# Optimization experiments

Hardware: AMD Instinct MI355X
Metric: run time of the kernel (lower is better)

The kernel has to match this reference:

```python
import jax, jax.numpy as jnp
import numpy as np
from jax import lax

B, T, MEL, D, H, NC = 8, 256, 128, 192, 4, 20
C_EVENT, C_SCENE = 8, 64
ETA, LR, ALPHA = 0.9, 0.1, 0.01  # memory momentum, write lr, forget rate
EPS = 1e-5


def _ln(x, g, b):
    m = x.mean(-1, keepdims=True)
    v = ((x - m) ** 2).mean(-1, keepdims=True)
    return (x - m) / jnp.sqrt(v + EPS) * g + b


def _mem_step(x, t, M, S, Wk, Wv, Wq, chunk):
    # x: [B,D]; M,S: [B,D,D]. Titans-style neural memory, updated every `chunk` steps.
    k = x @ Wk
    v = x @ Wv
    q = x @ Wq
    err = v - jnp.einsum('bd,bde->be', k, M)          # surprise / prediction error
    S_new = ETA * S + LR * jnp.einsum('bd,be->bde', k, err)
    M_new = (1.0 - ALPHA) * M + S_new
    upd = (t % chunk) == 0
    S = jnp.where(upd, S_new, S)
    M = jnp.where(upd, M_new, M)
    out = jnp.einsum('bd,bde->be', q, M)              # retrieval
    return out, M, S


def setup_inputs() -> dict:
    key = jax.random.key(0)
    ks = jax.random.split(key, 24)
    w = lambda k, shp, s=0.05: jax.random.normal(k, shp, dtype=jnp.float32) * s
    inp = {
        'x': jax.random.normal(ks[0], (B, T, MEL), dtype=jnp.float32),
        'W_in': w(ks[1], (MEL, D)), 'b_in': jnp.zeros((D,), jnp.float32),
        # MHA at seq_len=1: softmax over one key -> weight 1, so only V and out proj matter
        'Wv_a': w(ks[2], (D, D)), 'bv_a': jnp.zeros((D,), jnp.float32),
        'Wo_a': w(ks[3], (D, D)), 'bo_a': jnp.zeros((D,), jnp.float32),
        # conformer conv module (degenerate seq_len=1: depthwise conv -> center tap)
        'ln1_g': jnp.ones((D,), jnp.float32), 'ln1_b': jnp.zeros((D,), jnp.float32),
        'pw1_w': w(ks[4], (D, 2 * D)), 'pw1_b': jnp.zeros((2 * D,), jnp.float32),
        'dw_w': w(ks[5], (D,), 0.2), 'dw_b': jnp.zeros((D,), jnp.float32),
        'bn_s': jnp.ones((D,), jnp.float32), 'bn_b': jnp.zeros((D,), jnp.float32),
        'pw2_w': w(ks[6], (D, D)), 'pw2_b': jnp.zeros((D,), jnp.float32),
        # theta (event) / delta (scene) neural memory projections
        'Wk_t': w(ks[7], (D, D)), 'Wv_t': w(ks[8], (D, D)), 'Wq_t': w(ks[9], (D, D)),
        'Wk_d': w(ks[10], (D, D)), 'Wv_d': w(ks[11], (D, D)), 'Wq_d': w(ks[12], (D, D)),
        'ln2_g': jnp.ones((D,), jnp.float32), 'ln2_b': jnp.zeros((D,), jnp.float32),
        'Wc': w(ks[13], (D, NC)), 'bc': jnp.zeros((NC,), jnp.float32),
    }
    return inp


def reference(x, W_in, b_in, Wv_a, bv_a, Wo_a, bo_a, ln1_g, ln1_b, pw1_w, pw1_b,
              dw_w, dw_b, bn_s, bn_b, pw2_w, pw2_b, Wk_t, Wv_t, Wq_t,
              Wk_d, Wv_d, Wq_d, ln2_g, ln2_b, Wc, bc):
    xp = x @ W_in + b_in                               # [B,T,D]

    def step(carry, inp):
        x_t, t = inp                                   # x_t: [B,D]
        Mt, St, Md, Sd = carry
        d_out, Md, Sd = _mem_step(x_t, t, Md, Sd, Wk_d, Wv_d, Wq_d, C_SCENE)
        x1 = x_t + 0.5 * d_out
        attn = (x1 @ Wv_a + bv_a) @ Wo_a + bo_a        # single-token self-attn
        x2 = x1 + attn
        h = _ln(x2, ln1_g, ln1_b)
        h = h @ pw1_w + pw1_b
        a, g = jnp.split(h, 2, axis=-1)
        h = a * jax.nn.sigmoid(g)                      # GLU
        h = h * dw_w + dw_b                            # depthwise conv center tap
        h = h * bn_s + bn_b                            # eval-mode BN
        h = jax.nn.silu(h)
        h = h @ pw2_w + pw2_b
        x3 = x2 + h
        t_out, Mt, St = _mem_step(x3, t, Mt, St, Wk_t, Wv_t, Wq_t, C_EVENT)
        x4 = x3 + 0.5 * t_out
        return (Mt, St, Md, Sd), _ln(x4, ln2_g, ln2_b)

    z = jnp.zeros((B, D, D), jnp.float32)
    xs = (jnp.swapaxes(xp, 0, 1), jnp.arange(T))       # [T,B,D], [T]
    _, ys = lax.scan(step, (z, z, z, z), xs)
    y = jnp.swapaxes(ys, 0, 1)                         # [B,T,D]
    pooled = y.mean(axis=1)
    return pooled @ Wc + bc                            # [B,NC]
```

## Files before the change

### kernel.cpp

```cpp
#include <hip/hip_runtime.h>
#include <math.h>

#define Bb 8
#define Tt 256
#define MEL 128
#define Dd 192
#define NCc 20
#define ND 4
#define NT 32
#define ETAc 0.9f
#define LRc 0.1f
#define MDEC 0.99f
#define EPSc 1e-5f
#define PT 2
#define PTILES 128
#define RTT 4
#define PADD 196

__device__ __forceinline__ float sigmoidf_(float x) {
    return 1.0f / (1.0f + __expf(-x));
}

__device__ __forceinline__ float memcoef(int n, int i) {
    float m = LRc, pw = LRc;
    for (int nn = i + 1; nn <= n; nn++) { pw *= ETAc; m = MDEC * m + pw; }
    return m;
}

__device__ __forceinline__ float dot4(float4 a, float4 b) {
    return a.x * b.x + a.y * b.y + a.z * b.z + a.w * b.w;
}

__global__ __launch_bounds__(192) void prep(
    const float* __restrict__ Wv_a, const float* __restrict__ Wo_a,
    const float* __restrict__ bv_a, const float* __restrict__ bo_a,
    const float* __restrict__ Wq_t, const float* __restrict__ Wq_d,
    const float* __restrict__ x, const float* __restrict__ W_in,
    const float* __restrict__ b_in, const float* __restrict__ Wk_d,
    const float* __restrict__ Wv_d,
    float* __restrict__ Wavo_ws, float* __restrict__ b_avo,
    float* __restrict__ WqtT, float* __restrict__ WqdT,
    float* __restrict__ Kd_ws, float* __restrict__ Vd_ws,
    float* __restrict__ pooled)
{
    __shared__ __align__(16) float smem[768];
    int blk = blockIdx.x, tid = threadIdx.x;

    if (blk < 48) {
        int m0 = blk * 4;
        for (int q = tid; q < 4 * Dd; q += 192) smem[q] = Wv_a[m0 * Dd + q];
        __syncthreads();
        int o = tid;
        float a0 = 0.f, a1 = 0.f, a2 = 0.f, a3 = 0.f;
        #pragma unroll 4
        for (int k = 0; k < Dd; k += 2) {
            float w0 = Wo_a[(k + 0) * Dd + o], w1 = Wo_a[(k + 1) * Dd + o];
            a0 += w0 * smem[0 * Dd + k] + w1 * smem[0 * Dd + k + 1];
            a1 += w0 * smem[1 * Dd + k] + w1 * smem[1 * Dd + k + 1];
            a2 += w0 * smem[2 * Dd + k] + w1 * smem[2 * Dd + k + 1];
            a3 += w0 * smem[3 * Dd + k] + w1 * smem[3 * Dd + k + 1];
        }
        Wavo_ws[(m0 + 0) * Dd + o] = a0;
        Wavo_ws[(m0 + 1) * Dd + o] = a1;
        Wavo_ws[(m0 + 2) * Dd + o] = a2;
        Wavo_ws[(m0 + 3) * Dd + o] = a3;
        return;
    }
    if (blk == 48) {
        int o = tid;
        float s = bo_a[o];
        #pragma unroll 4
        for (int m = 0; m < Dd; m++) s += bv_a[m] * Wo_a[m * Dd + o];
        b_avo[o] = s;
        return;
    }
    if (blk < 97) {
        int r0 = 4 * (blk - 49);
        float4 v;
        v.x = Wq_t[(r0 + 0) * Dd + tid];
        v.y = Wq_t[(r0 + 1) * Dd + tid];
        v.z = Wq_t[(r0 + 2) * Dd + tid];
        v.w = Wq_t[(r0 + 3) * Dd + tid];
        *(float4*)&WqtT[tid * Dd + r0] = v;
        return;
    }
    if (blk < 145) {
        int r0 = 4 * (blk - 97);
        float4 v;
        v.x = Wq_d[(r0 + 0) * Dd + tid];
        v.y = Wq_d[(r0 + 1) * Dd + tid];
        v.z = Wq_d[(r0 + 2) * Dd + tid];
        v.w = Wq_d[(r0 + 3) * Dd + tid];
        *(float4*)&WqdT[tid * Dd + r0] = v;
        return;
    }
    if (blk == 177) {
        for (int q = tid; q < Bb * Dd; q += 192) pooled[q] = 0.f;
        return;
    }

    int q = blk - 145;
    int b = q >> 2, i = q & 3;
    float* XR = smem;
    float* XP = smem + 128;
    if (tid < 128) XR[tid] = x[((size_t)b * Tt + 64 * i) * MEL + tid];
    __syncthreads();
    {
        int o = tid;
        float acc = b_in[o];
        #pragma unroll 8
        for (int k = 0; k < MEL; k += 4) {
            acc += W_in[(k + 0) * Dd + o] * XR[k + 0];
            acc += W_in[(k + 1) * Dd + o] * XR[k + 1];
            acc += W_in[(k + 2) * Dd + o] * XR[k + 2];
            acc += W_in[(k + 3) * Dd + o] * XR[k + 3];
        }
        XP[o] = acc;
    }
    __syncthreads();
    {
        int o = tid;
        float ak = 0.f, av = 0.f;
        #pragma unroll 4
        for (int k = 0; k < Dd; k += 4) {
            float x0 = XP[k + 0], x1 = XP[k + 1], x2 = XP[k + 2], x3 = XP[k + 3];
            ak += Wk_d[(k + 0) * Dd + o] * x0 + Wk_d[(k + 1) * Dd + o] * x1
                + Wk_d[(k + 2) * Dd + o] * x2 + Wk_d[(k + 3) * Dd + o] * x3;
            av += Wv_d[(k + 0) * Dd + o] * x0 + Wv_d[(k + 1) * Dd + o] * x1
                + Wv_d[(k + 2) * Dd + o] * x2 + Wv_d[(k + 3) * Dd + o] * x3;
        }
        Kd_ws[(b * ND + i) * Dd + o] = ak;
        Vd_ws[(b * ND + i) * Dd + o] = av;
    }
}

__global__ __launch_bounds__(192) void delta_solve(
    const float* __restrict__ WqdT, const float* __restrict__ Kd_ws,
    float* __restrict__ Vd_ws, float* __restrict__ Ud_ws)
{
    int blk = blockIdx.x, b = blk / 5, role = blk % 5, tid = threadIdx.x;
    if (role == 0) {
        __shared__ __align__(16) float K4[ND][Dd], V4[ND][Dd];
        __shared__ float G[16], mc[16];
        for (int q = tid; q < ND * 48; q += 192) {
            int i = q / 48, c = q - i * 48;
            ((float4*)K4[i])[c] = ((const float4*)&Kd_ws[(b * ND + i) * Dd])[c];
            ((float4*)V4[i])[c] = ((const float4*)&Vd_ws[(b * ND + i) * Dd])[c];
        }
        __syncthreads();
        if (tid < 16) {
            int i = tid >> 2, j = tid & 3;
            float s = 0.f;
            for (int d = 0; d < Dd; d++) s += K4[i][d] * K4[j][d];
            G[tid] = s;
            mc[tid] = (j <= i) ? memcoef(i, j) : 0.f;
        }
        __syncthreads();
        for (int i = 1; i < ND; i++) {
            float acc = V4[i][tid];
            for (int m = 0; m < i; m++)
                acc -= mc[(i - 1) * ND + m] * G[i * ND + m] * V4[m][tid];
            V4[i][tid] = acc;
            __syncthreads();
        }
        for (int i = 0; i < ND; i++) Vd_ws[(b * ND + i) * Dd + tid] = V4[i][tid];
    } else {
        __shared__ float KS[Dd];
        int i = role - 1;
        KS[tid] = Kd_ws[(b * ND + i) * Dd + tid];
        __syncthreads();
        int o = tid;
        float acc = 0.f;
        #pragma unroll 8
        for (int k = 0; k < Dd; k += 4) {
            acc += WqdT[(k + 0) * Dd + o] * KS[k + 0];
            acc += WqdT[(k + 1) * Dd + o] * KS[k + 1];
            acc += WqdT[(k + 2) * Dd + o] * KS[k + 2];
            acc += WqdT[(k + 3) * Dd + o] * KS[k + 3];
        }
        Ud_ws[(b * ND + i) * Dd + o] = acc;
    }
}

__global__ __launch_bounds__(192) void pipeline(
    const float* __restrict__ x, const float* __restrict__ W_in,
    const float* __restrict__ b_in,
    const float* __restrict__ ln1_g, const float* __restrict__ ln1_b,
    const float* __restrict__ pw1_w, const float* __restrict__ pw1_b,
    const float* __restrict__ dw_w, const float* __restrict__ dw_b,
    const float* __restrict__ bn_s, const float* __restrict__ bn_b,
    const float* __restrict__ pw2_w, const float* __restrict__ pw2_b,
    const float* __restrict__ Wavo_ws, const float* __restrict__ b_avo,
    const float* __restrict__ Ed_ws, const float* __restrict__ Ud_ws,
    float* __restrict__ x3_ws)
{
    int blk = blockIdx.x;
    int b = blk >> 7, tile = blk & 127;
    int t0 = tile * PT, n = tile >> 5;
    int tid = threadIdx.x;

    __shared__ __align__(16) float XR[PT][MEL];
    __shared__ __align__(16) float XP[PT][Dd];
    __shared__ __align__(16) float ED[ND][PADD], UD[ND][PADD];
    __shared__ __align__(16) float X1[PT][Dd], X2[PT][Dd];
    __shared__ __align__(16) float LNX[PT][Dd], HG[PT][Dd];
    __shared__ float WQs[PT * ND];
    __shared__ float mv[PT][2];

    if (tid < PT * 32) {
        int r = tid >> 5, c = tid & 31;
        ((float4*)XR[r])[c] = ((const float4*)&x[((size_t)b * Tt + t0 + r) * MEL])[c];
    }
    for (int q = tid; q < ND * 48 * 2; q += 192) {
        int which = q >= ND * 48;
        int qq = which ? q - ND * 48 : q;
        int i = qq / 48, c = qq - i * 48;
        if (!which) ((float4*)ED[i])[c] = ((const float4*)&Ed_ws[(b * ND + i) * Dd])[c];
        else        ((float4*)UD[i])[c] = ((const float4*)&Ud_ws[(b * ND + i) * Dd])[c];
    }
    __syncthreads();

    int o = tid;
    {
        float acc[PT];
        float bb = b_in[o];
        #pragma unroll
        for (int r = 0; r < PT; r++) acc[r] = bb;
        #pragma unroll 8
        for (int k = 0; k < MEL; k += 4) {
            float w0 = W_in[(k + 0) * Dd + o], w1 = W_in[(k + 1) * Dd + o];
            float w2 = W_in[(k + 2) * Dd + o], w3 = W_in[(k + 3) * Dd + o];
            #pragma unroll
            for (int r = 0; r < PT; r++) {
                float4 xv = *(const float4*)&XR[r][k];
                acc[r] += w0 * xv.x + w1 * xv.y + w2 * xv.z + w3 * xv.w;
            }
        }
        #pragma unroll
        for (int r = 0; r < PT; r++) XP[r][tid] = acc[r];
    }
    __syncthreads();

    if (tid < PT * 32) {
        int r = tid >> 5, i = (tid >> 3) & 3, c = tid & 7;
        float s = 0.f;
        const float* xp = XP[r];
        const float* u = UD[i];
        #pragma unroll
        for (int j = 0; j < 24; j++) s += xp[c * 24 + j] * u[c * 24 + j];
        s += __shfl_down(s, 4, 8);
        s += __shfl_down(s, 2, 8);
        s += __shfl_down(s, 1, 8);
        if (c == 0) {
            float coef = (i <= n) ? memcoef(n, i) : 0.f;
            WQs[r * ND + i] = s * coef;
        }
    }
    __syncthreads();

    {
        #pragma unroll
        for (int r = 0; r < PT; r++) {
            float dout = WQs[r * ND + 0] * ED[0][tid] + WQs[r * ND + 1] * ED[1][tid]
                       + WQs[r * ND + 2] * ED[2][tid] + WQs[r * ND + 3] * ED[3][tid];
            X1[r][tid] = XP[r][tid] + 0.5f * dout;
        }
    }
    __syncthreads();

    {
        float acc[PT];
        float bb = b_avo[o];
        #pragma unroll
        for (int r = 0; r < PT; r++) acc[r] = bb;
        #pragma unroll 8
        for (int k = 0; k < Dd; k += 4) {
            float w0 = Wavo_ws[(k + 0) * Dd + o], w1 = Wavo_ws[(k + 1) * Dd + o];
            float w2 = Wavo_ws[(k + 2) * Dd + o], w3 = Wavo_ws[(k + 3) * Dd + o];
            #pragma unroll
            for (int r = 0; r < PT; r++) {
                float4 xv = *(const float4*)&X1[r][k];
                acc[r] += w0 * xv.x + w1 * xv.y + w2 * xv.z + w3 * xv.w;
            }
        }
        #pragma unroll
        for (int r = 0; r < PT; r++) X2[r][tid] = X1[r][tid] + acc[r];
    }
    __syncthreads();

    if (tid < PT * 32) {
        int r = tid >> 5, j = tid & 31;
        float s = 0.f, sq = 0.f;
        for (int d = j; d < Dd; d += 32) { float v = X2[r][d]; s += v; sq += v * v; }
        for (int off = 16; off > 0; off >>= 1) {
            s += __shfl_down(s, off, 32); sq += __shfl_down(sq, off, 32);
        }
        if (j == 0) {
            float mean = s / Dd;
            mv[r][0] = mean;
            mv[r][1] = rsqrtf(sq / Dd - mean * mean + EPSc);
        }
    }
    __syncthreads();
    {
        float g = ln1_g[tid], bb = ln1_b[tid];
        #pragma unroll
        for (int r = 0; r < PT; r++)
            LNX[r][tid] = (X2[r][tid] - mv[r][0]) * mv[r][1] * g + bb;
    }
    __syncthreads();

    {
        float aa[PT], gg[PT];
        float ba = pw1_b[o], bg = pw1_b[o + Dd];
        #pragma unroll
        for (int r = 0; r < PT; r++) { aa[r] = ba; gg[r] = bg; }
        #pragma unroll 4
        for (int k = 0; k < Dd; k += 4) {
            float wa0 = pw1_w[(k + 0) * 2 * Dd + o], wg0 = pw1_w[(k + 0) * 2 * Dd + Dd + o];
            float wa1 = pw1_w[(k + 1) * 2 * Dd + o], wg1 = pw1_w[(k + 1) * 2 * Dd + Dd + o];
            float wa2 = pw1_w[(k + 2) * 2 * Dd + o], wg2 = pw1_w[(k + 2) * 2 * Dd + Dd + o];
            float wa3 = pw1_w[(k + 3) * 2 * Dd + o], wg3 = pw1_w[(k + 3) * 2 * Dd + Dd + o];
            #pragma unroll
            for (int r = 0; r < PT; r++) {
                float4 xv = *(const float4*)&LNX[r][k];
                aa[r] += wa0 * xv.x + wa1 * xv.y + wa2 * xv.z + wa3 * xv.w;
                gg[r] += wg0 * xv.x + wg1 * xv.y + wg2 * xv.z + wg3 * xv.w;
            }
        }
        float dww = dw_w[o], dwb = dw_b[o], bns = bn_s[o], bnb = bn_b[o];
        #pragma unroll
        for (int r = 0; r < PT; r++) {
            float h = aa[r] * sigmoidf_(gg[r]);
            h = h * dww + dwb;
            h = h * bns + bnb;
            h = h * sigmoidf_(h);
            HG[r][tid] = h;
        }
    }
    __syncthreads();

    {
        float acc[PT];
        float bb = pw2_b[o];
        #pragma unroll
        for (int r = 0; r < PT; r++) acc[r] = bb;
        #pragma unroll 8
        for (int k = 0; k < Dd; k += 4) {
            float w0 = pw2_w[(k + 0) * Dd + o], w1 = pw2_w[(k + 1) * Dd + o];
            float w2 = pw2_w[(k + 2) * Dd + o], w3 = pw2_w[(k + 3) * Dd + o];
            #pragma unroll
            for (int r = 0; r < PT; r++) {
                float4 xv = *(const float4*)&HG[r][k];
                acc[r] += w0 * xv.x + w1 * xv.y + w2 * xv.z + w3 * xv.w;
            }
        }
        #pragma unroll
        for (int r = 0; r < PT; r++)
            x3_ws[((size_t)b * Tt + t0 + r) * Dd + tid] = X2[r][tid] + acc[r];
    }
}

__global__ __launch_bounds__(192) void theta_projU(
    const float* __restrict__ x3_ws,
    const float* __restrict__ Wk_t, const float* __restrict__ Wv_t,
    const float* __restrict__ WqtT,
    float* __restrict__ Kt_ws, float* __restrict__ Vt_ws,
    float* __restrict__ Ut_ws)
{
    int blk = blockIdx.x, b = blk >> 5, i = blk & 31;
    int tid = threadIdx.x;
    __shared__ float XS[Dd];
    __shared__ float KS[Dd];

    XS[tid] = x3_ws[((size_t)b * Tt + 8 * i) * Dd + tid];
    __syncthreads();

    int o = tid;
    float ak = 0.f, av = 0.f;
    #pragma unroll 4
    for (int k = 0; k < Dd; k += 4) {
        float x0 = XS[k + 0], x1 = XS[k + 1], x2 = XS[k + 2], x3 = XS[k + 3];
        ak += Wk_t[(k + 0) * Dd + o] * x0 + Wk_t[(k + 1) * Dd + o] * x1
            + Wk_t[(k + 2) * Dd + o] * x2 + Wk_t[(k + 3) * Dd + o] * x3;
        av += Wv_t[(k + 0) * Dd + o] * x0 + Wv_t[(k + 1) * Dd + o] * x1
            + Wv_t[(k + 2) * Dd + o] * x2 + Wv_t[(k + 3) * Dd + o] * x3;
    }
    Kt_ws[(b * NT + i) * Dd + o] = ak;
    Vt_ws[(b * NT + i) * Dd + o] = av;
    KS[o] = ak;
    __syncthreads();

    float au = 0.f;
    #pragma unroll 8
    for (int k = 0; k < Dd; k += 4) {
        au += WqtT[(k + 0) * Dd + o] * KS[k + 0];
        au += WqtT[(k + 1) * Dd + o] * KS[k + 1];
        au += WqtT[(k + 2) * Dd + o] * KS[k + 2];
        au += WqtT[(k + 3) * Dd + o] * KS[k + 3];
    }
    Ut_ws[(b * NT + i) * Dd + o] = au;
}

__global__ __launch_bounds__(192) void theta_solve(
    const float* __restrict__ Kt_ws, float* __restrict__ Vt_ws)
{
    int b = blockIdx.x, tid = threadIdx.x;
    __shared__ __align__(16) float K[NT][PADD];
    __shared__ float A[NT * NT], mc[NT * NT];

    for (int q = tid; q < NT * 48; q += 192) {
        int i = q / 48, c = q - i * 48;
        ((float4*)K[i])[c] = ((const float4*)&Kt_ws[(b * NT + i) * Dd])[c];
    }
    if (tid < NT) {
        int i = tid;
        float m = 0.f, pw = LRc;
        for (int nn = 0; nn < NT; nn++) {
            float v;
            if (nn < i) v = 0.f;
            else if (nn == i) { m = LRc; v = m; }
            else { pw *= ETAc; m = MDEC * m + pw; v = m; }
            mc[nn * NT + i] = v;
        }
    }
    __syncthreads();
    for (int p = tid; p < NT * NT; p += 192) {
        int i = p >> 5, j = p & 31;
        float s = 0.f;
        if (j < i) {
            const float4* ki = (const float4*)K[i];
            const float4* kj = (const float4*)K[j];
            float g = 0.f;
            #pragma unroll 4
            for (int kk = 0; kk < 48; kk++) g += dot4(ki[kk], kj[kk]);
            s = mc[(i - 1) * NT + j] * g;
        }
        A[p] = s;
    }
    __syncthreads();
    float e[NT];
    #pragma unroll
    for (int i = 0; i < NT; i++) e[i] = Vt_ws[(b * NT + i) * Dd + tid];
    #pragma unroll
    for (int i = 1; i < NT; i++) {
        float acc = e[i];
        #pragma unroll
        for (int m = 0; m < i; m++) acc -= A[i * NT + m] * e[m];
        e[i] = acc;
    }
    #pragma unroll
    for (int i = 0; i < NT; i++) Vt_ws[(b * NT + i) * Dd + tid] = e[i];
}

__global__ __launch_bounds__(256) void retrieve(
    const float* __restrict__ x3_ws, const float* __restrict__ Ut_ws,
    const float* __restrict__ Et_ws, const float* __restrict__ ln2_g,
    const float* __restrict__ ln2_b, float* __restrict__ pooled)
{
    int blk = blockIdx.x, b = blk >> 6, tile = blk & 63;
    int t0 = tile * RTT, n = tile >> 1;
    int tid = threadIdx.x;

    __shared__ __align__(16) float UT[NT][PADD];
    __shared__ __align__(16) float XS[RTT][PADD];
    __shared__ float WQ[RTT * NT];
    __shared__ float mv[RTT][2];

    for (int q = tid; q < NT * 48; q += 256) {
        int i = q / 48, c = q - i * 48;
        ((float4*)UT[i])[c] = ((const float4*)&Ut_ws[(b * NT + i) * Dd])[c];
    }
    for (int q = tid; q < RTT * 48; q += 256) {
        int r = q / 48, c = q - r * 48;
        ((float4*)XS[r])[c] = ((const float4*)&x3_ws[((size_t)b * Tt + t0 + r) * Dd])[c];
    }
    __syncthreads();

    {
        int r = tid >> 6, i = (tid >> 1) & 31, h = tid & 1;
        const float4* u4 = (const float4*)UT[i];
        const float4* x4 = (const float4*)XS[r];
        float s = 0.f;
        #pragma unroll 8
        for (int kk = h * 24; kk < h * 24 + 24; kk++) s += dot4(u4[kk], x4[kk]);
        s += __shfl_down(s, 1, 2);
        if (h == 0) {
            float coef = (i <= n) ? memcoef(n, i) : 0.f;
            WQ[r * NT + i] = s * coef;
        }
    }
    __syncthreads();

    if (tid < Dd) {
        float acc[RTT] = {};
        #pragma unroll 4
        for (int i = 0; i < NT; i++) {
            float e = Et_ws[(b * NT + i) * Dd + tid];
            #pragma unroll
            for (int r = 0; r < RTT; r++) acc[r] += WQ[r * NT + i] * e;
        }
        #pragma unroll
        for (int r = 0; r < RTT; r++) XS[r][tid] += 0.5f * acc[r];
    }
    __syncthreads();

    if (tid < RTT * 32) {
        int r = tid >> 5, j = tid & 31;
        float s = 0.f, sq = 0.f;
        for (int d = j; d < Dd; d += 32) { float v = XS[r][d]; s += v; sq += v * v; }
        for (int off = 16; off > 0; off >>= 1) {
            s += __shfl_down(s, off, 32); sq += __shfl_down(sq, off, 32);
        }
        if (j == 0) {
            float mean = s / Dd;
            mv[r][0] = mean;
            mv[r][1] = rsqrtf(sq / Dd - mean * mean + EPSc);
        }
    }
    __syncthreads();

    if (tid < Dd) {
        float g = ln2_g[tid], bb = ln2_b[tid];
        float sum = 0.f;
        #pragma unroll
        for (int r = 0; r < RTT; r++)
            sum += (XS[r][tid] - mv[r][0]) * mv[r][1] * g + bb;
        atomicAdd(&pooled[b * Dd + tid], sum);
    }
}

__global__ __launch_bounds__(192) void head(
    const float* __restrict__ pooled, const float* __restrict__ Wc,
    const float* __restrict__ bc, float* __restrict__ out)
{
    int tid = threadIdx.x;
    if (tid < Bb * NCc) {
        int b = tid / NCc, c = tid - b * NCc;
        float s = 0.f;
        for (int d = 0; d < Dd; d++) s += pooled[b * Dd + d] * Wc[d * NCc + c];
        out[tid] = s * (1.0f / Tt) + bc[c];
    }
}

extern "C" void kernel_launch(void* const* d_in, const int* in_sizes, int n_in,
                              void* d_out, int out_size, void* d_ws, size_t ws_size,
                              hipStream_t stream) {
    const float* x     = (const float*)d_in[0];
    const float* W_in  = (const float*)d_in[1];
    const float* b_in  = (const float*)d_in[2];
    const float* Wv_a  = (const float*)d_in[3];
    const float* bv_a  = (const float*)d_in[4];
    const float* Wo_a  = (const float*)d_in[5];
    const float* bo_a  = (const float*)d_in[6];
    const float* ln1_g = (const float*)d_in[7];
    const float* ln1_b = (const float*)d_in[8];
    const float* pw1_w = (const float*)d_in[9];
    const float* pw1_b = (const float*)d_in[10];
    const float* dw_w  = (const float*)d_in[11];
    const float* dw_b  = (const float*)d_in[12];
    const float* bn_s  = (const float*)d_in[13];
    const float* bn_b  = (const float*)d_in[14];
    const float* pw2_w = (const float*)d_in[15];
    const float* pw2_b = (const float*)d_in[16];
    const float* Wk_t  = (const float*)d_in[17];
    const float* Wv_t  = (const float*)d_in[18];
    const float* Wq_t  = (const float*)d_in[19];
    const float* Wk_d  = (const float*)d_in[20];
    const float* Wv_d  = (const float*)d_in[21];
    const float* Wq_d  = (const float*)d_in[22];
    const float* ln2_g = (const float*)d_in[23];
    const float* ln2_b = (const float*)d_in[24];
    const float* Wc    = (const float*)d_in[25];
    const float* bc    = (const float*)d_in[26];

    float* ws = (float*)d_ws;
    size_t off = 0;
    float* x3_ws   = ws + off; off += (size_t)Bb * Tt * Dd;
    float* Kd_ws   = ws + off; off += Bb * ND * Dd;
    float* Vd_ws   = ws + off; off += Bb * ND * Dd;
    float* Ud_ws   = ws + off; off += Bb * ND * Dd;
    float* Kt_ws   = ws + off; off += Bb * NT * Dd;
    float* Vt_ws   = ws + off; off += Bb * NT * Dd;
    float* Ut_ws   = ws + off; off += Bb * NT * Dd;
    float* pooled  = ws + off; off += Bb * Dd;
    float* Wavo_ws = ws + off; off += Dd * Dd;
    float* WqtT    = ws + off; off += Dd * Dd;
    float* WqdT    = ws + off; off += Dd * Dd;
    float* b_avo   = ws + off; off += Dd;

    prep<<<178, 192, 0, stream>>>(
        Wv_a, Wo_a, bv_a, bo_a, Wq_t, Wq_d,
        x, W_in, b_in, Wk_d, Wv_d,
        Wavo_ws, b_avo, WqtT, WqdT, Kd_ws, Vd_ws, pooled);
    delta_solve<<<Bb * 5, 192, 0, stream>>>(WqdT, Kd_ws, Vd_ws, Ud_ws);
    pipeline<<<Bb * PTILES, 192, 0, stream>>>(
        x, W_in, b_in, ln1_g, ln1_b, pw1_w, pw1_b, dw_w, dw_b,
        bn_s, bn_b, pw2_w, pw2_b, Wavo_ws, b_avo, Vd_ws, Ud_ws, x3_ws);
    theta_projU<<<Bb * NT, 192, 0, stream>>>(
        x3_ws, Wk_t, Wv_t, WqtT, Kt_ws, Vt_ws, Ut_ws);
    theta_solve<<<Bb, 192, 0, stream>>>(Kt_ws, Vt_ws);
    retrieve<<<Bb * 64, 256, 0, stream>>>(
        x3_ws, Ut_ws, Vt_ws, ln2_g, ln2_b, pooled);
    head<<<1, 192, 0, stream>>>(pooled, Wc, bc, (float*)d_out);
}
```

Before: 195.2 us.

## Split-K across two thread halves in pipeline and theta kernels, double rows per tile

```diff
diff --git a/kernel.cpp b/kernel.cpp
--- a/kernel.cpp
+++ b/kernel.cpp
@@ -12,8 +12,8 @@
 #define LRc 0.1f
 #define MDEC 0.99f
 #define EPSc 1e-5f
-#define PT 2
-#define PTILES 128
+#define PT 4
+#define PTILES 64
 #define RTT 4
 #define PADD 196
 
@@ -182,7 +182,7 @@
     }
 }
 
-__global__ __launch_bounds__(192) void pipeline(
+__global__ __launch_bounds__(384) void pipeline(
     const float* __restrict__ x, const float* __restrict__ W_in,
     const float* __restrict__ b_in,
     const float* __restrict__ ln1_g, const float* __restrict__ ln1_b,
@@ -195,15 +195,18 @@
     float* __restrict__ x3_ws)
 {
     int blk = blockIdx.x;
-    int b = blk >> 7, tile = blk & 127;
-    int t0 = tile * PT, n = tile >> 5;
+    int b = blk >> 6, tile = blk & 63;
+    int t0 = tile * PT, n = tile >> 4;
     int tid = threadIdx.x;
+    int h = (tid >= Dd) ? 1 : 0;
+    int o = tid - h * Dd;
 
     __shared__ __align__(16) float XR[PT][MEL];
     __shared__ __align__(16) float XP[PT][Dd];
     __shared__ __align__(16) float ED[ND][PADD], UD[ND][PADD];
     __shared__ __align__(16) float X1[PT][Dd], X2[PT][Dd];
     __shared__ __align__(16) float LNX[PT][Dd], HG[PT][Dd];
+    __shared__ __align__(16) float PS[PT][Dd];
     __shared__ float WQs[PT * ND];
     __shared__ float mv[PT][2];
 
@@ -211,7 +214,7 @@
         int r = tid >> 5, c = tid & 31;
         ((float4*)XR[r])[c] = ((const float4*)&x[((size_t)b * Tt + t0 + r) * MEL])[c];
     }
-    for (int q = tid; q < ND * 48 * 2; q += 192) {
+    for (int q = tid; q < ND * 48 * 2; q += 384) {
         int which = q >= ND * 48;
         int qq = which ? q - ND * 48 : q;
         int i = qq / 48, c = qq - i * 48;
@@ -220,14 +223,11 @@
     }
     __syncthreads();
 
-    int o = tid;
-    {
-        float acc[PT];
-        float bb = b_in[o];
-        #pragma unroll
-        for (int r = 0; r < PT; r++) acc[r] = bb;
-        #pragma unroll 8
-        for (int k = 0; k < MEL; k += 4) {
+    {
+        float acc[PT] = {0.f, 0.f, 0.f, 0.f};
+        int k0 = h * 64;
+        #pragma unroll 4
+        for (int k = k0; k < k0 + 64; k += 4) {
             float w0 = W_in[(k + 0) * Dd + o], w1 = W_in[(k + 1) * Dd + o];
             float w2 = W_in[(k + 2) * Dd + o], w3 = W_in[(k + 3) * Dd + o];
             #pragma unroll
@@ -236,10 +236,18 @@
                 acc[r] += w0 * xv.x + w1 * xv.y + w2 * xv.z + w3 * xv.w;
             }
         }
-        #pragma unroll
-        for (int r = 0; r < PT; r++) XP[r][tid] = acc[r];
-    }
-    __syncthreads();
+        if (h) {
+            #pragma unroll
+            for (int r = 0; r < PT; r++) PS[r][o] = acc[r];
+        }
+        __syncthreads();
+        if (!h) {
+            float bb = b_in[o];
+            #pragma unroll
+            for (int r = 0; r < PT; r++) XP[r][o] = acc[r] + PS[r][o] + bb;
+        }
+        __syncthreads();
+    }
 
     if (tid < PT * 32) {
         int r = tid >> 5, i = (tid >> 3) & 3, c = tid & 7;
@@ -260,21 +268,20 @@
 
     {
         #pragma unroll
-        for (int r = 0; r < PT; r++) {
-            float dout = WQs[r * ND + 0] * ED[0][tid] + WQs[r * ND + 1] * ED[1][tid]
-                       + WQs[r * ND + 2] * ED[2][tid] + WQs[r * ND + 3] * ED[3][tid];
-            X1[r][tid] = XP[r][tid] + 0.5f * dout;
-        }
-    }
-    __syncthreads();
-
-    {
-        float acc[PT];
-        float bb = b_avo[o];
-        #pragma unroll
-        for (int r = 0; r < PT; r++) acc[r] = bb;
-        #pragma unroll 8
-        for (int k = 0; k < Dd; k += 4) {
+        for (int rr = 0; rr < 2; rr++) {
+            int r = h * 2 + rr;
+            float dout = WQs[r * ND + 0] * ED[0][o] + WQs[r * ND + 1] * ED[1][o]
+                       + WQs[r * ND + 2] * ED[2][o] + WQs[r * ND + 3] * ED[3][o];
+            X1[r][o] = XP[r][o] + 0.5f * dout;
+        }
+    }
+    __syncthreads();
+
+    {
+        float acc[PT] = {0.f, 0.f, 0.f, 0.f};
+        int k0 = h * 96;
+        #pragma unroll 4
+        for (int k = k0; k < k0 + 96; k += 4) {
             float w0 = Wavo_ws[(k + 0) * Dd + o], w1 = Wavo_ws[(k + 1) * Dd + o];
             float w2 = Wavo_ws[(k + 2) * Dd + o], w3 = Wavo_ws[(k + 3) * Dd + o];
             #pragma unroll
@@ -283,10 +290,18 @@
                 acc[r] += w0 * xv.x + w1 * xv.y + w2 * xv.z + w3 * xv.w;
             }
         }
-        #pragma unroll
-        for (int r = 0; r < PT; r++) X2[r][tid] = X1[r][tid] + acc[r];
-    }
-    __syncthreads();
+        if (h) {
+            #pragma unroll
+            for (int r = 0; r < PT; r++) PS[r][o] = acc[r];
+        }
+        __syncthreads();
+        if (!h) {
+            float bb = b_avo[o];
+            #pragma unroll
+            for (int r = 0; r < PT; r++) X2[r][o] = X1[r][o] + acc[r] + PS[r][o] + bb;
+        }
+        __syncthreads();
+    }
 
     if (tid < PT * 32) {
         int r = tid >> 5, j = tid & 31;
@@ -303,50 +318,55 @@
     }
     __syncthreads();
     {
-        float g = ln1_g[tid], bb = ln1_b[tid];
-        #pragma unroll
-        for (int r = 0; r < PT; r++)
-            LNX[r][tid] = (X2[r][tid] - mv[r][0]) * mv[r][1] * g + bb;
-    }
-    __syncthreads();
-
-    {
-        float aa[PT], gg[PT];
-        float ba = pw1_b[o], bg = pw1_b[o + Dd];
-        #pragma unroll
-        for (int r = 0; r < PT; r++) { aa[r] = ba; gg[r] = bg; }
+        float g = ln1_g[o], bb = ln1_b[o];
+        #pragma unroll
+        for (int rr = 0; rr < 2; rr++) {
+            int r = h * 2 + rr;
+            LNX[r][o] = (X2[r][o] - mv[r][0]) * mv[r][1] * g + bb;
+        }
+    }
+    __syncthreads();
+
+    {
+        int oc = h ? (Dd + o) : o;
+        float acc[PT];
+        float bb = pw1_b[oc];
+        #pragma unroll
+        for (int r = 0; r < PT; r++) acc[r] = bb;
         #pragma unroll 4
         for (int k = 0; k < Dd; k += 4) {
-            float wa0 = pw1_w[(k + 0) * 2 * Dd + o], wg0 = pw1_w[(k + 0) * 2 * Dd + Dd + o];
-            float wa1 = pw1_w[(k + 1) * 2 * Dd + o], wg1 = pw1_w[(k + 1) * 2 * Dd + Dd + o];
-            float wa2 = pw1_w[(k + 2) * 2 * Dd + o], wg2 = pw1_w[(k + 2) * 2 * Dd + Dd + o];
-            float wa3 = pw1_w[(k + 3) * 2 * Dd + o], wg3 = pw1_w[(k + 3) * 2 * Dd + Dd + o];
+            float w0 = pw1_w[(k + 0) * 2 * Dd + oc], w1 = pw1_w[(k + 1) * 2 * Dd + oc];
+            float w2 = pw1_w[(k + 2) * 2 * Dd + oc], w3 = pw1_w[(k + 3) * 2 * Dd + oc];
             #pragma unroll
             for (int r = 0; r < PT; r++) {
                 float4 xv = *(const float4*)&LNX[r][k];
-                aa[r] += wa0 * xv.x + wa1 * xv.y + wa2 * xv.z + wa3 * xv.w;
-                gg[r] += wg0 * xv.x + wg1 * xv.y + wg2 * xv.z + wg3 * xv.w;
+                acc[r] += w0 * xv.x + w1 * xv.y + w2 * xv.z + w3 * xv.w;
             }
         }
-        float dww = dw_w[o], dwb = dw_b[o], bns = bn_s[o], bnb = bn_b[o];
-        #pragma unroll
-        for (int r = 0; r < PT; r++) {
-            float h = aa[r] * sigmoidf_(gg[r]);
-            h = h * dww + dwb;
-            h = h * bns + bnb;
-            h = h * sigmoidf_(h);
-            HG[r][tid] = h;
-        }
-    }
-    __syncthreads();
-
-    {
-        float acc[PT];
-        float bb = pw2_b[o];
-        #pragma unroll
-        for (int r = 0; r < PT; r++) acc[r] = bb;
-        #pragma unroll 8
-        for (int k = 0; k < Dd; k += 4) {
+        if (h) {
+            #pragma unroll
+            for (int r = 0; r < PT; r++) PS[r][o] = acc[r];
+        }
+        __syncthreads();
+        if (!h) {
+            float dww = dw_w[o], dwb = dw_b[o], bns = bn_s[o], bnb = bn_b[o];
+            #pragma unroll
+            for (int r = 0; r < PT; r++) {
+                float hh = acc[r] * sigmoidf_(PS[r][o]);
+                hh = hh * dww + dwb;
+                hh = hh * bns + bnb;
+                hh = hh * sigmoidf_(hh);
+                HG[r][o] = hh;
+            }
+        }
+        __syncthreads();
+    }
+
+    {
+        float acc[PT] = {0.f, 0.f, 0.f, 0.f};
+        int k0 = h * 96;
+        #pragma unroll 4
+        for (int k = k0; k < k0 + 96; k += 4) {
             float w0 = pw2_w[(k + 0) * Dd + o], w1 = pw2_w[(k + 1) * Dd + o];
             float w2 = pw2_w[(k + 2) * Dd + o], w3 = pw2_w[(k + 3) * Dd + o];
             #pragma unroll
@@ -355,13 +375,21 @@
                 acc[r] += w0 * xv.x + w1 * xv.y + w2 * xv.z + w3 * xv.w;
             }
         }
-        #pragma unroll
-        for (int r = 0; r < PT; r++)
-            x3_ws[((size_t)b * Tt + t0 + r) * Dd + tid] = X2[r][tid] + acc[r];
-    }
-}
-
-__global__ __launch_bounds__(192) void theta_projU(
+        if (h) {
+            #pragma unroll
+            for (int r = 0; r < PT; r++) PS[r][o] = acc[r];
+        }
+        __syncthreads();
+        if (!h) {
+            float bb = pw2_b[o];
+            #pragma unroll
+            for (int r = 0; r < PT; r++)
+                x3_ws[((size_t)b * Tt + t0 + r) * Dd + o] = X2[r][o] + acc[r] + PS[r][o] + bb;
+        }
+    }
+}
+
+__global__ __launch_bounds__(384) void theta_projU(
     const float* __restrict__ x3_ws,
     const float* __restrict__ Wk_t, const float* __restrict__ Wv_t,
     const float* __restrict__ WqtT,
@@ -370,46 +398,47 @@
 {
     int blk = blockIdx.x, b = blk >> 5, i = blk & 31;
     int tid = threadIdx.x;
-    __shared__ float XS[Dd];
-    __shared__ float KS[Dd];
-
-    XS[tid] = x3_ws[((size_t)b * Tt + 8 * i) * Dd + tid];
-    __syncthreads();
-
-    int o = tid;
-    float ak = 0.f, av = 0.f;
+    int h = (tid >= Dd) ? 1 : 0;
+    int o = tid - h * Dd;
+    __shared__ __align__(16) float XS[Dd];
+    __shared__ __align__(16) float KS[Dd];
+    __shared__ __align__(16) float PS[Dd];
+
+    if (tid < 48)
+        ((float4*)XS)[tid] = ((const float4*)&x3_ws[((size_t)b * Tt + 8 * i) * Dd])[tid];
+    __syncthreads();
+
+    const float* W = h ? Wv_t : Wk_t;
+    float a = 0.f;
     #pragma unroll 4
     for (int k = 0; k < Dd; k += 4) {
-        float x0 = XS[k + 0], x1 = XS[k + 1], x2 = XS[k + 2], x3 = XS[k + 3];
-        ak += Wk_t[(k + 0) * Dd + o] * x0 + Wk_t[(k + 1) * Dd + o] * x1
-            + Wk_t[(k + 2) * Dd + o] * x2 + Wk_t[(k + 3) * Dd + o] * x3;
-        av += Wv_t[(k + 0) * Dd + o] * x0 + Wv_t[(k + 1) * Dd + o] * x1
-            + Wv_t[(k + 2) * Dd + o] * x2 + Wv_t[(k + 3) * Dd + o] * x3;
-    }
-    Kt_ws[(b * NT + i) * Dd + o] = ak;
-    Vt_ws[(b * NT + i) * Dd + o] = av;
-    KS[o] = ak;
+        a += W[(k + 0) * Dd + o] * XS[k + 0] + W[(k + 1) * Dd + o] * XS[k + 1]
+           + W[(k + 2) * Dd + o] * XS[k + 2] + W[(k + 3) * Dd + o] * XS[k + 3];
+    }
+    if (!h) { Kt_ws[(b * NT + i) * Dd + o] = a; KS[o] = a; }
+    else    { Vt_ws[(b * NT + i) * Dd + o] = a; }
     __syncthreads();
 
     float au = 0.f;
-    #pragma unroll 8
-    for (int k = 0; k < Dd; k += 4) {
-        au += WqtT[(k + 0) * Dd + o] * KS[k + 0];
-        au += WqtT[(k + 1) * Dd + o] * KS[k + 1];
-        au += WqtT[(k + 2) * Dd + o] * KS[k + 2];
-        au += WqtT[(k + 3) * Dd + o] * KS[k + 3];
-    }
-    Ut_ws[(b * NT + i) * Dd + o] = au;
-}
-
-__global__ __launch_bounds__(192) void theta_solve(
+    int k0 = h * 96;
+    #pragma unroll 4
+    for (int k = k0; k < k0 + 96; k += 4) {
+        au += WqtT[(k + 0) * Dd + o] * KS[k + 0] + WqtT[(k + 1) * Dd + o] * KS[k + 1]
+            + WqtT[(k + 2) * Dd + o] * KS[k + 2] + WqtT[(k + 3) * Dd + o] * KS[k + 3];
+    }
+    if (h) PS[o] = au;
+    __syncthreads();
+    if (!h) Ut_ws[(b * NT + i) * Dd + o] = au + PS[o];
+}
+
+__global__ __launch_bounds__(512) void theta_solve(
     const float* __restrict__ Kt_ws, float* __restrict__ Vt_ws)
 {
     int b = blockIdx.x, tid = threadIdx.x;
     __shared__ __align__(16) float K[NT][PADD];
     __shared__ float A[NT * NT], mc[NT * NT];
 
-    for (int q = tid; q < NT * 48; q += 192) {
+    for (int q = tid; q < NT * 48; q += 512) {
         int i = q / 48, c = q - i * 48;
         ((float4*)K[i])[c] = ((const float4*)&Kt_ws[(b * NT + i) * Dd])[c];
     }
@@ -425,7 +454,7 @@
         }
     }
     __syncthreads();
-    for (int p = tid; p < NT * NT; p += 192) {
+    for (int p = tid; p < NT * NT; p += 512) {
         int i = p >> 5, j = p & 31;
         float s = 0.f;
         if (j < i) {
@@ -439,18 +468,20 @@
         A[p] = s;
     }
     __syncthreads();
-    float e[NT];
-    #pragma unroll
-    for (int i = 0; i < NT; i++) e[i] = Vt_ws[(b * NT + i) * Dd + tid];
-    #pragma unroll
-    for (int i = 1; i < NT; i++) {
-        float acc = e[i];
-        #pragma unroll
-        for (int m = 0; m < i; m++) acc -= A[i * NT + m] * e[m];
-        e[i] = acc;
-    }
-    #pragma unroll
-    for (int i = 0; i < NT; i++) Vt_ws[(b * NT + i) * Dd + tid] = e[i];
+    if (tid < Dd) {
+        float e[NT];
+        #pragma unroll
+        for (int i = 0; i < NT; i++) e[i] = Vt_ws[(b * NT + i) * Dd + tid];
+        #pragma unroll
+        for (int i = 1; i < NT; i++) {
+            float acc = e[i];
+            #pragma unroll
+            for (int m = 0; m < i; m++) acc -= A[i * NT + m] * e[m];
+            e[i] = acc;
+        }
+        #pragma unroll
+        for (int i = 0; i < NT; i++) Vt_ws[(b * NT + i) * Dd + tid] = e[i];
+    }
 }
 
 __global__ __launch_bounds__(256) void retrieve(
@@ -594,12 +625,12 @@
         x, W_in, b_in, Wk_d, Wv_d,
         Wavo_ws, b_avo, WqtT, WqdT, Kd_ws, Vd_ws, pooled);
     delta_solve<<<Bb * 5, 192, 0, stream>>>(WqdT, Kd_ws, Vd_ws, Ud_ws);
-    pipeline<<<Bb * PTILES, 192, 0, stream>>>(
+    pipeline<<<Bb * PTILES, 384, 0, stream>>>(
         x, W_in, b_in, ln1_g, ln1_b, pw1_w, pw1_b, dw_w, dw_b,
         bn_s, bn_b, pw2_w, pw2_b, Wavo_ws, b_avo, Vd_ws, Ud_ws, x3_ws);
-    theta_projU<<<Bb * NT, 192, 0, stream>>>(
+    theta_projU<<<Bb * NT, 384, 0, stream>>>(
         x3_ws, Wk_t, Wv_t, WqtT, Kt_ws, Vt_ws, Ut_ws);
-    theta_solve<<<Bb, 192, 0, stream>>>(Kt_ws, Vt_ws);
+    theta_solve<<<Bb, 512, 0, stream>>>(Kt_ws, Vt_ws);
     retrieve<<<Bb * 64, 256, 0, stream>>>(
         x3_ws, Ut_ws, Vt_ws, ln2_g, ln2_b, pooled);
     head<<<1, 192, 0, stream>>>(pooled, Wc, bc, (float*)d_out);
```

Result: slower. 204.2 us (+4.6%).

## Fuse theta solve and head into preceding kernels via last-block atomic counters

Applied to the files above, without the earlier changes.

```diff
diff --git a/kernel.cpp b/kernel.cpp
--- a/kernel.cpp
+++ b/kernel.cpp
@@ -41,7 +41,7 @@
     float* __restrict__ Wavo_ws, float* __restrict__ b_avo,
     float* __restrict__ WqtT, float* __restrict__ WqdT,
     float* __restrict__ Kd_ws, float* __restrict__ Vd_ws,
-    float* __restrict__ pooled)
+    float* __restrict__ pooled, unsigned int* __restrict__ cnt)
 {
     __shared__ __align__(16) float smem[768];
     int blk = blockIdx.x, tid = threadIdx.x;
@@ -96,6 +96,7 @@
     }
     if (blk == 177) {
         for (int q = tid; q < Bb * Dd; q += 192) pooled[q] = 0.f;
+        if (tid < 12) cnt[tid] = 0u;
         return;
     }
 
@@ -361,102 +362,109 @@
     }
 }
 
-__global__ __launch_bounds__(192) void theta_projU(
+__global__ __launch_bounds__(384) void theta_projU_solve(
     const float* __restrict__ x3_ws,
     const float* __restrict__ Wk_t, const float* __restrict__ Wv_t,
     const float* __restrict__ WqtT,
     float* __restrict__ Kt_ws, float* __restrict__ Vt_ws,
-    float* __restrict__ Ut_ws)
+    float* __restrict__ Ut_ws, unsigned int* __restrict__ cnt)
 {
     int blk = blockIdx.x, b = blk >> 5, i = blk & 31;
     int tid = threadIdx.x;
-    __shared__ float XS[Dd];
-    __shared__ float KS[Dd];
-
-    XS[tid] = x3_ws[((size_t)b * Tt + 8 * i) * Dd + tid];
-    __syncthreads();
-
-    int o = tid;
-    float ak = 0.f, av = 0.f;
+    int h = (tid >= Dd) ? 1 : 0;
+    int o = tid - h * Dd;
+    __shared__ __align__(16) float XS[Dd];
+    __shared__ __align__(16) float KS[Dd];
+    __shared__ __align__(16) float PS[Dd];
+
+    if (tid < 48)
+        ((float4*)XS)[tid] = ((const float4*)&x3_ws[((size_t)b * Tt + 8 * i) * Dd])[tid];
+    __syncthreads();
+
+    const float* W = h ? Wv_t : Wk_t;
+    float a = 0.f;
     #pragma unroll 4
     for (int k = 0; k < Dd; k += 4) {
-        float x0 = XS[k + 0], x1 = XS[k + 1], x2 = XS[k + 2], x3 = XS[k + 3];
-        ak += Wk_t[(k + 0) * Dd + o] * x0 + Wk_t[(k + 1) * Dd + o] * x1
-            + Wk_t[(k + 2) * Dd + o] * x2 + Wk_t[(k + 3) * Dd + o] * x3;
-        av += Wv_t[(k + 0) * Dd + o] * x0 + Wv_t[(k + 1) * Dd + o] * x1
-            + Wv_t[(k + 2) * Dd + o] * x2 + Wv_t[(k + 3) * Dd + o] * x3;
-    }
-    Kt_ws[(b * NT + i) * Dd + o] = ak;
-    Vt_ws[(b * NT + i) * Dd + o] = av;
-    KS[o] = ak;
+        a += W[(k + 0) * Dd + o] * XS[k + 0] + W[(k + 1) * Dd + o] * XS[k + 1]
+           + W[(k + 2) * Dd + o] * XS[k + 2] + W[(k + 3) * Dd + o] * XS[k + 3];
+    }
+    if (!h) { Kt_ws[(b * NT + i) * Dd + o] = a; KS[o] = a; }
+    else    { Vt_ws[(b * NT + i) * Dd + o] = a; }
     __syncthreads();
 
     float au = 0.f;
-    #pragma unroll 8
-    for (int k = 0; k < Dd; k += 4) {
-        au += WqtT[(k + 0) * Dd + o] * KS[k + 0];
-        au += WqtT[(k + 1) * Dd + o] * KS[k + 1];
-        au += WqtT[(k + 2) * Dd + o] * KS[k + 2];
-        au += WqtT[(k + 3) * Dd + o] * KS[k + 3];
-    }
-    Ut_ws[(b * NT + i) * Dd + o] = au;
-}
-
-__global__ __launch_bounds__(192) void theta_solve(
-    const float* __restrict__ Kt_ws, float* __restrict__ Vt_ws)
-{
-    int b = blockIdx.x, tid = threadIdx.x;
+    int k0 = h * 96;
+    #pragma unroll 4
+    for (int k = k0; k < k0 + 96; k += 4) {
+        au += WqtT[(k + 0) * Dd + o] * KS[k + 0] + WqtT[(k + 1) * Dd + o] * KS[k + 1]
+            + WqtT[(k + 2) * Dd + o] * KS[k + 2] + WqtT[(k + 3) * Dd + o] * KS[k + 3];
+    }
+    if (h) PS[o] = au;
+    __syncthreads();
+    if (!h) Ut_ws[(b * NT + i) * Dd + o] = au + PS[o];
+
+    __syncthreads();
+    __shared__ unsigned int sdone;
+    if (tid == 0) { __threadfence(); sdone = atomicAdd(&cnt[b], 1u); }
+    __syncthreads();
+    if (sdone != 31u) return;
+    __threadfence();
+
     __shared__ __align__(16) float K[NT][PADD];
     __shared__ float A[NT * NT], mc[NT * NT];
 
-    for (int q = tid; q < NT * 48; q += 192) {
-        int i = q / 48, c = q - i * 48;
-        ((float4*)K[i])[c] = ((const float4*)&Kt_ws[(b * NT + i) * Dd])[c];
+    for (int q = tid; q < NT * 48; q += 384) {
+        int ii = q / 48, c = q - ii * 48;
+        ((float4*)K[ii])[c] = ((const float4*)&Kt_ws[(b * NT + ii) * Dd])[c];
     }
     if (tid < NT) {
-        int i = tid;
+        int ii = tid;
         float m = 0.f, pw = LRc;
         for (int nn = 0; nn < NT; nn++) {
             float v;
-            if (nn < i) v = 0.f;
-            else if (nn == i) { m = LRc; v = m; }
+            if (nn < ii) v = 0.f;
+            else if (nn == ii) { m = LRc; v = m; }
             else { pw *= ETAc; m = MDEC * m + pw; v = m; }
-            mc[nn * NT + i] = v;
-        }
-    }
-    __syncthreads();
-    for (int p = tid; p < NT * NT; p += 192) {
-        int i = p >> 5, j = p & 31;
+            mc[nn * NT + ii] = v;
+        }
+    }
+    __syncthreads();
+    for (int p = tid; p < NT * NT; p += 384) {
+        int ii = p >> 5, j = p & 31;
         float s = 0.f;
-        if (j < i) {
-            const float4* ki = (const float4*)K[i];
+        if (j < ii) {
+            const float4* ki = (const float4*)K[ii];
             const float4* kj = (const float4*)K[j];
             float g = 0.f;
             #pragma unroll 4
             for (int kk = 0; kk < 48; kk++) g += dot4(ki[kk], kj[kk]);
-            s = mc[(i - 1) * NT + j] * g;
+            s = mc[(ii - 1) * NT + j] * g;
         }
         A[p] = s;
     }
     __syncthreads();
-    float e[NT];
-    #pragma unroll
-    for (int i = 0; i < NT; i++) e[i] = Vt_ws[(b * NT + i) * Dd + tid];
-    #pragma unroll
-    for (int i = 1; i < NT; i++) {
-        float acc = e[i];
-        #pragma unroll
-        for (int m = 0; m < i; m++) acc -= A[i * NT + m] * e[m];
-        e[i] = acc;
-    }
-    #pragma unroll
-    for (int i = 0; i < NT; i++) Vt_ws[(b * NT + i) * Dd + tid] = e[i];
+    if (tid < Dd) {
+        float e[NT];
+        #pragma unroll
+        for (int ii = 0; ii < NT; ii++) e[ii] = Vt_ws[(b * NT + ii) * Dd + tid];
+        #pragma unroll
+        for (int ii = 1; ii < NT; ii++) {
+            float acc = e[ii];
+            #pragma unroll
+            for (int m = 0; m < ii; m++) acc -= A[ii * NT + m] * e[m];
+            e[ii] = acc;
+        }
+        #pragma unroll
+        for (int ii = 0; ii < NT; ii++) Vt_ws[(b * NT + ii) * Dd + tid] = e[ii];
+    }
 }
 
 __global__ __launch_bounds__(256) void retrieve(
     const float* __restrict__ x3_ws, const float* __restrict__ Ut_ws,
     const float* __restrict__ Et_ws, const float* __restrict__ ln2_g,
-    const float* __restrict__ ln2_b, float* __restrict__ pooled)
+    const float* __restrict__ ln2_b, float* __restrict__ pooled,
+    const float* __restrict__ Wc, const float* __restrict__ bc,
+    float* __restrict__ out, unsigned int* __restrict__ cnt)
 {
     int blk = blockIdx.x, b = blk >> 6, tile = blk & 63;
     int t0 = tile * RTT, n = tile >> 1;
@@ -528,17 +536,18 @@
             sum += (XS[r][tid] - mv[r][0]) * mv[r][1] * g + bb;
         atomicAdd(&pooled[b * Dd + tid], sum);
     }
-}
-
-__global__ __launch_bounds__(192) void head(
-    const float* __restrict__ pooled, const float* __restrict__ Wc,
-    const float* __restrict__ bc, float* __restrict__ out)
-{
-    int tid = threadIdx.x;
+
+    __syncthreads();
+    __shared__ unsigned int sdone;
+    if (tid == 0) { __threadfence(); sdone = atomicAdd(&cnt[8], 1u); }
+    __syncthreads();
+    if (sdone != (unsigned)(Bb * 64 - 1)) return;
+    __threadfence();
+
     if (tid < Bb * NCc) {
-        int b = tid / NCc, c = tid - b * NCc;
+        int b2 = tid / NCc, c = tid - b2 * NCc;
         float s = 0.f;
-        for (int d = 0; d < Dd; d++) s += pooled[b * Dd + d] * Wc[d * NCc + c];
+        for (int d = 0; d < Dd; d++) s += pooled[b2 * Dd + d] * Wc[d * NCc + c];
         out[tid] = s * (1.0f / Tt) + bc[c];
     }
 }
@@ -588,19 +597,18 @@
     float* WqtT    = ws + off; off += Dd * Dd;
     float* WqdT    = ws + off; off += Dd * Dd;
     float* b_avo   = ws + off; off += Dd;
+    unsigned int* cnt = (unsigned int*)(ws + off); off += 16;
 
     prep<<<178, 192, 0, stream>>>(
         Wv_a, Wo_a, bv_a, bo_a, Wq_t, Wq_d,
         x, W_in, b_in, Wk_d, Wv_d,
-        Wavo_ws, b_avo, WqtT, WqdT, Kd_ws, Vd_ws, pooled);
+        Wavo_ws, b_avo, WqtT, WqdT, Kd_ws, Vd_ws, pooled, cnt);
     delta_solve<<<Bb * 5, 192, 0, stream>>>(WqdT, Kd_ws, Vd_ws, Ud_ws);
     pipeline<<<Bb * PTILES, 192, 0, stream>>>(
         x, W_in, b_in, ln1_g, ln1_b, pw1_w, pw1_b, dw_w, dw_b,
         bn_s, bn_b, pw2_w, pw2_b, Wavo_ws, b_avo, Vd_ws, Ud_ws, x3_ws);
-    theta_projU<<<Bb * NT, 192, 0, stream>>>(
-        x3_ws, Wk_t, Wv_t, WqtT, Kt_ws, Vt_ws, Ut_ws);
-    theta_solve<<<Bb, 192, 0, stream>>>(Kt_ws, Vt_ws);
+    theta_projU_solve<<<Bb * NT, 384, 0, stream>>>(
+        x3_ws, Wk_t, Wv_t, WqtT, Kt_ws, Vt_ws, Ut_ws, cnt);
     retrieve<<<Bb * 64, 256, 0, stream>>>(
-        x3_ws, Ut_ws, Vt_ws, ln2_g, ln2_b, pooled);
-    head<<<1, 192, 0, stream>>>(pooled, Wc, bc, (float*)d_out);
-}
+        x3_ws, Ut_ws, Vt_ws, ln2_g, ln2_b, pooled, Wc, bc, (float*)d_out, cnt);
+}
```

Measured after the change: 202.0 us. 1.03x slower.

## Fuse theta projections into pipeline kernel and widen solve blocks

Applied to the files above, without the earlier changes.

```diff
diff --git a/kernel.cpp b/kernel.cpp
--- a/kernel.cpp
+++ b/kernel.cpp
@@ -148,11 +148,19 @@
             ((float4*)V4[i])[c] = ((const float4*)&Vd_ws[(b * ND + i) * Dd])[c];
         }
         __syncthreads();
+        if (tid < 128) {
+            int p = tid >> 3, c = tid & 7;
+            int i = p >> 2, j = p & 3;
+            float s = 0.f;
+            #pragma unroll
+            for (int d = c * 24; d < c * 24 + 24; d++) s += K4[i][d] * K4[j][d];
+            s += __shfl_down(s, 4, 8);
+            s += __shfl_down(s, 2, 8);
+            s += __shfl_down(s, 1, 8);
+            if (c == 0) G[p] = s;
+        }
         if (tid < 16) {
             int i = tid >> 2, j = tid & 3;
-            float s = 0.f;
-            for (int d = 0; d < Dd; d++) s += K4[i][d] * K4[j][d];
-            G[tid] = s;
             mc[tid] = (j <= i) ? memcoef(i, j) : 0.f;
         }
         __syncthreads();
@@ -192,7 +200,11 @@
     const float* __restrict__ pw2_w, const float* __restrict__ pw2_b,
     const float* __restrict__ Wavo_ws, const float* __restrict__ b_avo,
     const float* __restrict__ Ed_ws, const float* __restrict__ Ud_ws,
-    float* __restrict__ x3_ws)
+    const float* __restrict__ Wk_t, const float* __restrict__ Wv_t,
+    const float* __restrict__ WqtT,
+    float* __restrict__ x3_ws,
+    float* __restrict__ Kt_ws, float* __restrict__ Vt_ws,
+    float* __restrict__ Ut_ws)
 {
     int blk = blockIdx.x;
     int b = blk >> 7, tile = blk & 127;
@@ -340,6 +352,7 @@
     }
     __syncthreads();
 
+    float x3v0;
     {
         float acc[PT];
         float bb = pw2_b[o];
@@ -358,58 +371,50 @@
         #pragma unroll
         for (int r = 0; r < PT; r++)
             x3_ws[((size_t)b * Tt + t0 + r) * Dd + tid] = X2[r][tid] + acc[r];
-    }
-}
-
-__global__ __launch_bounds__(192) void theta_projU(
-    const float* __restrict__ x3_ws,
-    const float* __restrict__ Wk_t, const float* __restrict__ Wv_t,
-    const float* __restrict__ WqtT,
-    float* __restrict__ Kt_ws, float* __restrict__ Vt_ws,
-    float* __restrict__ Ut_ws)
-{
-    int blk = blockIdx.x, b = blk >> 5, i = blk & 31;
-    int tid = threadIdx.x;
-    __shared__ float XS[Dd];
-    __shared__ float KS[Dd];
-
-    XS[tid] = x3_ws[((size_t)b * Tt + 8 * i) * Dd + tid];
-    __syncthreads();
-
-    int o = tid;
-    float ak = 0.f, av = 0.f;
-    #pragma unroll 4
-    for (int k = 0; k < Dd; k += 4) {
-        float x0 = XS[k + 0], x1 = XS[k + 1], x2 = XS[k + 2], x3 = XS[k + 3];
-        ak += Wk_t[(k + 0) * Dd + o] * x0 + Wk_t[(k + 1) * Dd + o] * x1
-            + Wk_t[(k + 2) * Dd + o] * x2 + Wk_t[(k + 3) * Dd + o] * x3;
-        av += Wv_t[(k + 0) * Dd + o] * x0 + Wv_t[(k + 1) * Dd + o] * x1
-            + Wv_t[(k + 2) * Dd + o] * x2 + Wv_t[(k + 3) * Dd + o] * x3;
-    }
-    Kt_ws[(b * NT + i) * Dd + o] = ak;
-    Vt_ws[(b * NT + i) * Dd + o] = av;
-    KS[o] = ak;
-    __syncthreads();
-
-    float au = 0.f;
-    #pragma unroll 8
-    for (int k = 0; k < Dd; k += 4) {
-        au += WqtT[(k + 0) * Dd + o] * KS[k + 0];
-        au += WqtT[(k + 1) * Dd + o] * KS[k + 1];
-        au += WqtT[(k + 2) * Dd + o] * KS[k + 2];
-        au += WqtT[(k + 3) * Dd + o] * KS[k + 3];
-    }
-    Ut_ws[(b * NT + i) * Dd + o] = au;
-}
-
-__global__ __launch_bounds__(192) void theta_solve(
+        x3v0 = X2[0][tid] + acc[0];
+    }
+
+    if ((tile & 3) == 0) {
+        int i = tile >> 2;
+        float* XS = LNX[0];
+        float* KS = LNX[1];
+        XS[tid] = x3v0;
+        __syncthreads();
+
+        float ak = 0.f, av = 0.f;
+        #pragma unroll 4
+        for (int k = 0; k < Dd; k += 4) {
+            float x0 = XS[k + 0], x1 = XS[k + 1], x2 = XS[k + 2], x3 = XS[k + 3];
+            ak += Wk_t[(k + 0) * Dd + o] * x0 + Wk_t[(k + 1) * Dd + o] * x1
+                + Wk_t[(k + 2) * Dd + o] * x2 + Wk_t[(k + 3) * Dd + o] * x3;
+            av += Wv_t[(k + 0) * Dd + o] * x0 + Wv_t[(k + 1) * Dd + o] * x1
+                + Wv_t[(k + 2) * Dd + o] * x2 + Wv_t[(k + 3) * Dd + o] * x3;
+        }
+        Kt_ws[(b * NT + i) * Dd + o] = ak;
+        Vt_ws[(b * NT + i) * Dd + o] = av;
+        KS[o] = ak;
+        __syncthreads();
+
+        float au = 0.f;
+        #pragma unroll 8
+        for (int k = 0; k < Dd; k += 4) {
+            au += WqtT[(k + 0) * Dd + o] * KS[k + 0];
+            au += WqtT[(k + 1) * Dd + o] * KS[k + 1];
+            au += WqtT[(k + 2) * Dd + o] * KS[k + 2];
+            au += WqtT[(k + 3) * Dd + o] * KS[k + 3];
+        }
+        Ut_ws[(b * NT + i) * Dd + o] = au;
+    }
+}
+
+__global__ __launch_bounds__(512) void theta_solve(
     const float* __restrict__ Kt_ws, float* __restrict__ Vt_ws)
 {
     int b = blockIdx.x, tid = threadIdx.x;
     __shared__ __align__(16) float K[NT][PADD];
     __shared__ float A[NT * NT], mc[NT * NT];
 
-    for (int q = tid; q < NT * 48; q += 192) {
+    for (int q = tid; q < NT * 48; q += 512) {
         int i = q / 48, c = q - i * 48;
         ((float4*)K[i])[c] = ((const float4*)&Kt_ws[(b * NT + i) * Dd])[c];
     }
@@ -425,7 +430,7 @@
         }
     }
     __syncthreads();
-    for (int p = tid; p < NT * NT; p += 192) {
+    for (int p = tid; p < NT * NT; p += 512) {
         int i = p >> 5, j = p & 31;
         float s = 0.f;
         if (j < i) {
@@ -439,18 +444,20 @@
         A[p] = s;
     }
     __syncthreads();
-    float e[NT];
-    #pragma unroll
-    for (int i = 0; i < NT; i++) e[i] = Vt_ws[(b * NT + i) * Dd + tid];
-    #pragma unroll
-    for (int i = 1; i < NT; i++) {
-        float acc = e[i];
-        #pragma unroll
-        for (int m = 0; m < i; m++) acc -= A[i * NT + m] * e[m];
-        e[i] = acc;
-    }
-    #pragma unroll
-    for (int i = 0; i < NT; i++) Vt_ws[(b * NT + i) * Dd + tid] = e[i];
+    if (tid < Dd) {
+        float e[NT];
+        #pragma unroll
+        for (int i = 0; i < NT; i++) e[i] = Vt_ws[(b * NT + i) * Dd + tid];
+        #pragma unroll
+        for (int i = 1; i < NT; i++) {
+            float acc = e[i];
+            #pragma unroll
+            for (int m = 0; m < i; m++) acc -= A[i * NT + m] * e[m];
+            e[i] = acc;
+        }
+        #pragma unroll
+        for (int i = 0; i < NT; i++) Vt_ws[(b * NT + i) * Dd + tid] = e[i];
+    }
 }
 
 __global__ __launch_bounds__(256) void retrieve(
@@ -596,10 +603,9 @@
     delta_solve<<<Bb * 5, 192, 0, stream>>>(WqdT, Kd_ws, Vd_ws, Ud_ws);
     pipeline<<<Bb * PTILES, 192, 0, stream>>>(
         x, W_in, b_in, ln1_g, ln1_b, pw1_w, pw1_b, dw_w, dw_b,
-        bn_s, bn_b, pw2_w, pw2_b, Wavo_ws, b_avo, Vd_ws, Ud_ws, x3_ws);
-    theta_projU<<<Bb * NT, 192, 0, stream>>>(
-        x3_ws, Wk_t, Wv_t, WqtT, Kt_ws, Vt_ws, Ut_ws);
-    theta_solve<<<Bb, 192, 0, stream>>>(Kt_ws, Vt_ws);
+        bn_s, bn_b, pw2_w, pw2_b, Wavo_ws, b_avo, Vd_ws, Ud_ws,
+        Wk_t, Wv_t, WqtT, x3_ws, Kt_ws, Vt_ws, Ut_ws);
+    theta_solve<<<Bb, 512, 0, stream>>>(Kt_ws, Vt_ws);
     retrieve<<<Bb * 64, 256, 0, stream>>>(
         x3_ws, Ut_ws, Vt_ws, ln2_g, ln2_b, pooled);
     head<<<1, 192, 0, stream>>>(pooled, Wc, bc, (float*)d_out);
```

Result: faster. 189.2 us (-3.1%).
